# Optimization experiments

Measured on AMD Instinct MI355X. Metric: run time of the kernel, lower is better.

Reference implementation:

```python
import jax, jax.numpy as jnp
import numpy as np

H = 1024  # hid_dim


def setup_inputs() -> dict:
    key = jax.random.key(0)
    k1, k2, k3, k4 = jax.random.split(key, 4)
    B, S = 64, 2048
    dec_out = jax.random.normal(k1, (B, H), dtype=jnp.float32)
    enc_outs = jax.random.normal(k2, (S, B, H), dtype=jnp.float32)
    # GeneralScorer W_a: Linear(H, H, bias=False); torch Linear: y = x @ W.T
    W_a = jax.random.normal(k3, (H, H), dtype=jnp.float32) / np.sqrt(H)
    # linear_out: Linear(2H, H, bias=False) since scorer == 'general'
    W_out = jax.random.normal(k4, (H, 2 * H), dtype=jnp.float32) / np.sqrt(2 * H)
    return {"dec_out": dec_out, "enc_outs": enc_outs, "W_a": W_a, "W_out": W_out}


def reference(dec_out, enc_outs, W_a, W_out):
    # GeneralScorer: project query then dot with each encoder state
    q = dec_out @ W_a.T                               # [B, H]
    scores = jnp.einsum('sbh,bh->bs', enc_outs, q)    # [B, S]
    weights = jax.nn.softmax(scores, axis=1)          # [B, S]
    # context = weights @ enc_outs (per batch)
    context = jnp.einsum('bs,sbh->bh', weights, enc_outs)  # [B, H]
    context = jnp.tanh(jnp.concatenate([context, dec_out], axis=1) @ W_out.T)
    return (context, weights)
```

## Files before the change

### kernel.cpp

```cpp
#include <hip/hip_runtime.h>
#include <math.h>

#define BB 64
#define SS 2048
#define HH 1024
#define NCHUNK 16
#define CHUNK 128

#define Q_OFF    0
#define PCTX_OFF (BB * HH)
#define PML_OFF  (PCTX_OFF + BB * NCHUNK * HH)
#define CTXF_OFF (PML_OFF + BB * NCHUNK * 2)

__global__ __launch_bounds__(256) void gemm64(
    const float* __restrict__ A0, const float* __restrict__ A1,
    const float* __restrict__ W, float* __restrict__ out,
    int nchunks, int do_tanh)
{
    __shared__ float A_lds[64 * 256];
    __shared__ float W_lds[4 * 256];
    const int t  = threadIdx.x;
    const int it = blockIdx.x;
    const int b  = t & 63;
    const int il = t >> 6;
    const int K  = nchunks << 8;
    float acc = 0.f;

    for (int kc = 0; kc < nchunks; ++kc) {
        for (int idx = t; idx < 64 * 64; idx += 256) {
            const int row = idx >> 6;
            const int g   = idx & 63;
            const float* src = (kc < 4) ? (A0 + row * 1024 + kc * 256)
                                        : (A1 + row * 1024 + (kc - 4) * 256);
            float4 v = *(const float4*)(src + g * 4);
            ((float4*)A_lds)[row * 64 + (g ^ row)] = v;
        }
        for (int idx = t; idx < 1024; idx += 256) {
            const int r2 = idx >> 8;
            const int cc = idx & 255;
            W_lds[idx] = W[(size_t)(it * 4 + r2) * K + kc * 256 + cc];
        }
        __syncthreads();
        #pragma unroll 8
        for (int j4 = 0; j4 < 64; ++j4) {
            float4 a  = ((const float4*)A_lds)[b * 64 + (j4 ^ b)];
            float4 wv = ((const float4*)W_lds)[il * 64 + j4];
            acc += a.x * wv.x + a.y * wv.y + a.z * wv.z + a.w * wv.w;
        }
        __syncthreads();
    }
    if (do_tanh) acc = tanhf(acc);
    out[b * 1024 + it * 4 + il] = acc;
}

__global__ __launch_bounds__(256) void attn_partial(
    const float* __restrict__ enc, const float* __restrict__ q,
    float* __restrict__ part_ctx, float* __restrict__ part_ml,
    float* __restrict__ scores_raw)
{
    __shared__ float q_lds[HH];
    __shared__ float ctx_lds[4][HH];
    __shared__ float ml_lds[4][2];

    const int t = threadIdx.x;
    const int c = blockIdx.x;
    const int b = blockIdx.y;

    for (int i = t; i < HH / 4; i += 256)
        ((float4*)q_lds)[i] = ((const float4*)(q + b * HH))[i];
    __syncthreads();

    const int w    = t >> 6;
    const int lane = t & 63;
    float m = -INFINITY, lsum = 0.f;
    float ctx[16];
    #pragma unroll
    for (int e = 0; e < 16; ++e) ctx[e] = 0.f;

    const int RPW = CHUNK / 4;
    for (int r = 0; r < RPW; ++r) {
        const int s = c * CHUNK + w * RPW + r;
        const float* row = enc + ((size_t)s * BB + b) * HH;
        float4 v[4];
        float partial = 0.f;
        #pragma unroll
        for (int k = 0; k < 4; ++k) {
            v[k] = *(const float4*)(row + k * 256 + 4 * lane);
            float4 qv = *(const float4*)(q_lds + k * 256 + 4 * lane);
            partial += v[k].x * qv.x + v[k].y * qv.y + v[k].z * qv.z + v[k].w * qv.w;
        }
        #pragma unroll
        for (int off = 32; off; off >>= 1)
            partial += __shfl_xor(partial, off, 64);
        const float sc = partial;
        if (lane == 0) scores_raw[b * SS + s] = sc;

        if (sc > m) {
            const float scale = expf(m - sc);
            lsum *= scale;
            #pragma unroll
            for (int e = 0; e < 16; ++e) ctx[e] *= scale;
            m = sc;
        }
        const float p = expf(sc - m);
        lsum += p;
        #pragma unroll
        for (int k = 0; k < 4; ++k) {
            ctx[4 * k + 0] += p * v[k].x;
            ctx[4 * k + 1] += p * v[k].y;
            ctx[4 * k + 2] += p * v[k].z;
            ctx[4 * k + 3] += p * v[k].w;
        }
    }

    if (lane == 0) { ml_lds[w][0] = m; ml_lds[w][1] = lsum; }
    #pragma unroll
    for (int k = 0; k < 4; ++k)
        *(float4*)&ctx_lds[w][k * 256 + 4 * lane] =
            make_float4(ctx[4 * k + 0], ctx[4 * k + 1], ctx[4 * k + 2], ctx[4 * k + 3]);
    __syncthreads();

    const float m0 = ml_lds[0][0], m1 = ml_lds[1][0], m2 = ml_lds[2][0], m3 = ml_lds[3][0];
    const float mb = fmaxf(fmaxf(m0, m1), fmaxf(m2, m3));
    const float f0 = expf(m0 - mb), f1 = expf(m1 - mb), f2 = expf(m2 - mb), f3 = expf(m3 - mb);
    const float lb = f0 * ml_lds[0][1] + f1 * ml_lds[1][1] + f2 * ml_lds[2][1] + f3 * ml_lds[3][1];

    float4 a0 = ((const float4*)&ctx_lds[0][0])[t];
    float4 a1 = ((const float4*)&ctx_lds[1][0])[t];
    float4 a2 = ((const float4*)&ctx_lds[2][0])[t];
    float4 a3 = ((const float4*)&ctx_lds[3][0])[t];
    float4 o;
    o.x = f0 * a0.x + f1 * a1.x + f2 * a2.x + f3 * a3.x;
    o.y = f0 * a0.y + f1 * a1.y + f2 * a2.y + f3 * a3.y;
    o.z = f0 * a0.z + f1 * a1.z + f2 * a2.z + f3 * a3.z;
    o.w = f0 * a0.w + f1 * a1.w + f2 * a2.w + f3 * a3.w;
    ((float4*)(part_ctx + ((size_t)b * NCHUNK + c) * HH))[t] = o;
    if (t == 0) {
        part_ml[(b * NCHUNK + c) * 2 + 0] = mb;
        part_ml[(b * NCHUNK + c) * 2 + 1] = lb;
    }
}

__global__ __launch_bounds__(256) void attn_combine(
    const float* __restrict__ part_ctx, const float* __restrict__ part_ml,
    float* __restrict__ ctx_final, float* __restrict__ wts)
{
    const int b = blockIdx.x;
    const int t = threadIdx.x;
    __shared__ float mls[NCHUNK][2];
    for (int i = t; i < NCHUNK * 2; i += 256)
        ((float*)mls)[i] = part_ml[b * NCHUNK * 2 + i];
    __syncthreads();

    float M = -INFINITY;
    #pragma unroll
    for (int c2 = 0; c2 < NCHUNK; ++c2) M = fmaxf(M, mls[c2][0]);
    float f[NCHUNK];
    float L = 0.f;
    #pragma unroll
    for (int c2 = 0; c2 < NCHUNK; ++c2) {
        f[c2] = expf(mls[c2][0] - M);
        L += f[c2] * mls[c2][1];
    }
    const float inv = 1.0f / L;

    float4 acc = make_float4(0.f, 0.f, 0.f, 0.f);
    #pragma unroll
    for (int c2 = 0; c2 < NCHUNK; ++c2) {
        float4 v = ((const float4*)(part_ctx + ((size_t)b * NCHUNK + c2) * HH))[t];
        acc.x += f[c2] * v.x; acc.y += f[c2] * v.y;
        acc.z += f[c2] * v.z; acc.w += f[c2] * v.w;
    }
    acc.x *= inv; acc.y *= inv; acc.z *= inv; acc.w *= inv;
    ((float4*)(ctx_final + (size_t)b * HH))[t] = acc;

    for (int s = t; s < SS; s += 256)
        wts[b * SS + s] = expf(wts[b * SS + s] - M) * inv;
}

extern "C" void kernel_launch(void* const* d_in, const int* in_sizes, int n_in,
                              void* d_out, int out_size, void* d_ws, size_t ws_size,
                              hipStream_t stream)
{
    const float* dec   = (const float*)d_in[0];
    const float* enc   = (const float*)d_in[1];
    const float* W_a   = (const float*)d_in[2];
    const float* W_out = (const float*)d_in[3];
    float* out = (float*)d_out;
    float* ws  = (float*)d_ws;

    float* q         = ws + Q_OFF;
    float* part_ctx  = ws + PCTX_OFF;
    float* part_ml   = ws + PML_OFF;
    float* ctx_final = ws + CTXF_OFF;
    float* wts       = out + BB * HH;

    gemm64<<<256, 256, 0, stream>>>(dec, dec, W_a, q, 4, 0);
    attn_partial<<<dim3(NCHUNK, BB), 256, 0, stream>>>(enc, q, part_ctx, part_ml, wts);
    attn_combine<<<BB, 256, 0, stream>>>(part_ctx, part_ml, ctx_final, wts);
    gemm64<<<256, 256, 0, stream>>>(ctx_final, dec, W_out, out, 8, 1);
}
```

Before: 208.5 us.

## Split-K GEMMs, double-buffer encoder loads, and widen attention chunking

Both GEMMs move to a split-K kernel in which each thread computes four output columns. Partial sums go to workspace and are reduced in the attention kernel and in a new tanh combine kernel. The attention partial kernel now uses 32 chunks of 64 rows, processes two rows per step with register double-buffered nontemporal loads and a branchless online softmax, and the combine kernel is spread over four blocks per batch. The aim is more parallelism and better hiding of memory latency on the dominant encoder stream, at the cost of an extra launch and extra workspace traffic for the partial results.

```diff
diff --git a/kernel.cpp b/kernel.cpp
--- a/kernel.cpp
+++ b/kernel.cpp
@@ -4,57 +4,67 @@
 #define BB 64
 #define SS 2048
 #define HH 1024
-#define NCHUNK 16
-#define CHUNK 128
-
-#define Q_OFF    0
-#define PCTX_OFF (BB * HH)
+#define NCHUNK 32
+#define CHUNK 64
+#define RPW 16
+
+typedef float f4 __attribute__((ext_vector_type(4)));
+
+#define QP_OFF   0
+#define PCTX_OFF (QP_OFF + 4 * BB * HH)
 #define PML_OFF  (PCTX_OFF + BB * NCHUNK * HH)
 #define CTXF_OFF (PML_OFF + BB * NCHUNK * 2)
-
-__global__ __launch_bounds__(256) void gemm64(
+#define OP_OFF   (CTXF_OFF + BB * HH)
+
+__global__ __launch_bounds__(256) void gemm_cols16(
     const float* __restrict__ A0, const float* __restrict__ A1,
-    const float* __restrict__ W, float* __restrict__ out,
-    int nchunks, int do_tanh)
-{
-    __shared__ float A_lds[64 * 256];
-    __shared__ float W_lds[4 * 256];
-    const int t  = threadIdx.x;
-    const int it = blockIdx.x;
-    const int b  = t & 63;
-    const int il = t >> 6;
-    const int K  = nchunks << 8;
-    float acc = 0.f;
-
-    for (int kc = 0; kc < nchunks; ++kc) {
-        for (int idx = t; idx < 64 * 64; idx += 256) {
-            const int row = idx >> 6;
-            const int g   = idx & 63;
-            const float* src = (kc < 4) ? (A0 + row * 1024 + kc * 256)
-                                        : (A1 + row * 1024 + (kc - 4) * 256);
-            float4 v = *(const float4*)(src + g * 4);
-            ((float4*)A_lds)[row * 64 + (g ^ row)] = v;
-        }
-        for (int idx = t; idx < 1024; idx += 256) {
-            const int r2 = idx >> 8;
-            const int cc = idx & 255;
-            W_lds[idx] = W[(size_t)(it * 4 + r2) * K + kc * 256 + cc];
+    const float* __restrict__ W, float* __restrict__ out_part,
+    int KTOT, int CPB)
+{
+    __shared__ f4 A_lds[64 * 32];
+    __shared__ f4 W_lds[16 * 32];
+    const int t    = threadIdx.x;
+    const int tile = blockIdx.x;
+    const int spl  = blockIdx.y;
+    const int b    = t & 63;
+    const int cg   = t >> 6;
+    float acc[4] = {0.f, 0.f, 0.f, 0.f};
+
+    for (int kk = 0; kk < CPB; ++kk) {
+        const int kc = spl * CPB + kk;
+        #pragma unroll
+        for (int i = 0; i < 8; ++i) {
+            const int idx = t + i * 256;
+            const int row = idx >> 5, g = idx & 31;
+            const float* src = (kc < 8) ? (A0 + row * 1024 + kc * 128)
+                                        : (A1 + row * 1024 + (kc - 8) * 128);
+            A_lds[row * 32 + (g ^ (row & 31))] = *(const f4*)(src + g * 4);
+        }
+        #pragma unroll
+        for (int i = 0; i < 2; ++i) {
+            const int idx = t + i * 256;
+            const int r = idx >> 5, g = idx & 31;
+            W_lds[r * 32 + g] =
+                *(const f4*)(W + (size_t)(tile * 16 + r) * KTOT + kc * 128 + g * 4);
         }
         __syncthreads();
         #pragma unroll 8
-        for (int j4 = 0; j4 < 64; ++j4) {
-            float4 a  = ((const float4*)A_lds)[b * 64 + (j4 ^ b)];
-            float4 wv = ((const float4*)W_lds)[il * 64 + j4];
-            acc += a.x * wv.x + a.y * wv.y + a.z * wv.z + a.w * wv.w;
+        for (int j4 = 0; j4 < 32; ++j4) {
+            const f4 a = A_lds[b * 32 + (j4 ^ (b & 31))];
+            #pragma unroll
+            for (int cix = 0; cix < 4; ++cix) {
+                const f4 wv = W_lds[(cg * 4 + cix) * 32 + j4];
+                acc[cix] += a.x * wv.x + a.y * wv.y + a.z * wv.z + a.w * wv.w;
+            }
         }
         __syncthreads();
     }
-    if (do_tanh) acc = tanhf(acc);
-    out[b * 1024 + it * 4 + il] = acc;
-}
-
-__global__ __launch_bounds__(256) void attn_partial(
-    const float* __restrict__ enc, const float* __restrict__ q,
+    float* op = out_part + ((size_t)spl * BB + b) * HH + tile * 16 + cg * 4;
+    *(f4*)op = (f4){acc[0], acc[1], acc[2], acc[3]};
+}
+
+__global__ __launch_bounds__(256, 4) void attn_partial(
+    const float* __restrict__ enc, const float* __restrict__ qp,
     float* __restrict__ part_ctx, float* __restrict__ part_ml,
     float* __restrict__ scores_raw)
 {
@@ -66,58 +76,80 @@
     const int c = blockIdx.x;
     const int b = blockIdx.y;
 
-    for (int i = t; i < HH / 4; i += 256)
-        ((float4*)q_lds)[i] = ((const float4*)(q + b * HH))[i];
+    {
+        const f4 v = ((const f4*)(qp + (size_t)b * HH))[t]
+                   + ((const f4*)(qp + 65536 + (size_t)b * HH))[t]
+                   + ((const f4*)(qp + 131072 + (size_t)b * HH))[t]
+                   + ((const f4*)(qp + 196608 + (size_t)b * HH))[t];
+        ((f4*)q_lds)[t] = v;
+    }
     __syncthreads();
 
     const int w    = t >> 6;
     const int lane = t & 63;
+    const size_t RS = (size_t)BB * HH;
+    const float* rp = enc + ((size_t)(c * CHUNK + w * RPW) * BB + b) * HH + 4 * lane;
+
+    f4 cur0[4], cur1[4], nxt0[4], nxt1[4];
+    #pragma unroll
+    for (int k = 0; k < 4; ++k) {
+        cur0[k] = __builtin_nontemporal_load((const f4*)(rp + k * 256));
+        cur1[k] = __builtin_nontemporal_load((const f4*)(rp + RS + k * 256));
+    }
+
     float m = -INFINITY, lsum = 0.f;
-    float ctx[16];
-    #pragma unroll
-    for (int e = 0; e < 16; ++e) ctx[e] = 0.f;
-
-    const int RPW = CHUNK / 4;
-    for (int r = 0; r < RPW; ++r) {
-        const int s = c * CHUNK + w * RPW + r;
-        const float* row = enc + ((size_t)s * BB + b) * HH;
-        float4 v[4];
-        float partial = 0.f;
+    f4 ctxv[4];
+    #pragma unroll
+    for (int k = 0; k < 4; ++k) ctxv[k] = (f4)0.f;
+
+    #pragma unroll
+    for (int r = 0; r < RPW; r += 2) {
+        if (r + 2 < RPW) {
+            const float* np = rp + 2 * RS;
+            #pragma unroll
+            for (int k = 0; k < 4; ++k) {
+                nxt0[k] = __builtin_nontemporal_load((const f4*)(np + k * 256));
+                nxt1[k] = __builtin_nontemporal_load((const f4*)(np + RS + k * 256));
+            }
+        }
+        float d0 = 0.f, d1 = 0.f;
         #pragma unroll
         for (int k = 0; k < 4; ++k) {
-            v[k] = *(const float4*)(row + k * 256 + 4 * lane);
-            float4 qv = *(const float4*)(q_lds + k * 256 + 4 * lane);
-            partial += v[k].x * qv.x + v[k].y * qv.y + v[k].z * qv.z + v[k].w * qv.w;
-        }
-        #pragma unroll
-        for (int off = 32; off; off >>= 1)
-            partial += __shfl_xor(partial, off, 64);
-        const float sc = partial;
-        if (lane == 0) scores_raw[b * SS + s] = sc;
-
-        if (sc > m) {
-            const float scale = expf(m - sc);
-            lsum *= scale;
+            const f4 qv = *(const f4*)(q_lds + k * 256 + 4 * lane);
+            d0 += cur0[k].x * qv.x + cur0[k].y * qv.y + cur0[k].z * qv.z + cur0[k].w * qv.w;
+            d1 += cur1[k].x * qv.x + cur1[k].y * qv.y + cur1[k].z * qv.z + cur1[k].w * qv.w;
+        }
+        #pragma unroll
+        for (int off = 32; off; off >>= 1) {
+            d0 += __shfl_xor(d0, off, 64);
+            d1 += __shfl_xor(d1, off, 64);
+        }
+        if (lane == 0) {
+            const int s = c * CHUNK + w * RPW + r;
+            scores_raw[b * SS + s]     = d0;
+            scores_raw[b * SS + s + 1] = d1;
+        }
+        const float mx = fmaxf(d0, d1);
+        const float nm = fmaxf(m, mx);
+        const float sc = expf(m - nm);
+        const float p0 = expf(d0 - nm);
+        const float p1 = expf(d1 - nm);
+        lsum = lsum * sc + p0 + p1;
+        m = nm;
+        #pragma unroll
+        for (int k = 0; k < 4; ++k)
+            ctxv[k] = ctxv[k] * sc + p0 * cur0[k] + p1 * cur1[k];
+        if (r + 2 < RPW) {
             #pragma unroll
-            for (int e = 0; e < 16; ++e) ctx[e] *= scale;
-            m = sc;
-        }
-        const float p = expf(sc - m);
-        lsum += p;
-        #pragma unroll
-        for (int k = 0; k < 4; ++k) {
-            ctx[4 * k + 0] += p * v[k].x;
-            ctx[4 * k + 1] += p * v[k].y;
-            ctx[4 * k + 2] += p * v[k].z;
-            ctx[4 * k + 3] += p * v[k].w;
+            for (int k = 0; k < 4; ++k) { cur0[k] = nxt0[k]; cur1[k] = nxt1[k]; }
+            rp += 2 * RS;
         }
     }
 
     if (lane == 0) { ml_lds[w][0] = m; ml_lds[w][1] = lsum; }
     #pragma unroll
     for (int k = 0; k < 4; ++k)
-        *(float4*)&ctx_lds[w][k * 256 + 4 * lane] =
-            make_float4(ctx[4 * k + 0], ctx[4 * k + 1], ctx[4 * k + 2], ctx[4 * k + 3]);
+        *(f4*)&ctx_lds[w][k * 256 + 4 * lane] = ctxv[k];
     __syncthreads();
 
     const float m0 = ml_lds[0][0], m1 = ml_lds[1][0], m2 = ml_lds[2][0], m3 = ml_lds[3][0];
@@ -125,16 +157,12 @@
     const float f0 = expf(m0 - mb), f1 = expf(m1 - mb), f2 = expf(m2 - mb), f3 = expf(m3 - mb);
     const float lb = f0 * ml_lds[0][1] + f1 * ml_lds[1][1] + f2 * ml_lds[2][1] + f3 * ml_lds[3][1];
 
-    float4 a0 = ((const float4*)&ctx_lds[0][0])[t];
-    float4 a1 = ((const float4*)&ctx_lds[1][0])[t];
-    float4 a2 = ((const float4*)&ctx_lds[2][0])[t];
-    float4 a3 = ((const float4*)&ctx_lds[3][0])[t];
-    float4 o;
-    o.x = f0 * a0.x + f1 * a1.x + f2 * a2.x + f3 * a3.x;
-    o.y = f0 * a0.y + f1 * a1.y + f2 * a2.y + f3 * a3.y;
-    o.z = f0 * a0.z + f1 * a1.z + f2 * a2.z + f3 * a3.z;
-    o.w = f0 * a0.w + f1 * a1.w + f2 * a2.w + f3 * a3.w;
-    ((float4*)(part_ctx + ((size_t)b * NCHUNK + c) * HH))[t] = o;
+    const f4 a0 = ((const f4*)&ctx_lds[0][0])[t];
+    const f4 a1 = ((const f4*)&ctx_lds[1][0])[t];
+    const f4 a2 = ((const f4*)&ctx_lds[2][0])[t];
+    const f4 a3 = ((const f4*)&ctx_lds[3][0])[t];
+    const f4 o = f0 * a0 + f1 * a1 + f2 * a2 + f3 * a3;
+    ((f4*)(part_ctx + ((size_t)(b * NCHUNK + c)) * HH))[t] = o;
     if (t == 0) {
         part_ml[(b * NCHUNK + c) * 2 + 0] = mb;
         part_ml[(b * NCHUNK + c) * 2 + 1] = lb;
@@ -145,37 +173,49 @@
     const float* __restrict__ part_ctx, const float* __restrict__ part_ml,
     float* __restrict__ ctx_final, float* __restrict__ wts)
 {
-    const int b = blockIdx.x;
-    const int t = threadIdx.x;
-    __shared__ float mls[NCHUNK][2];
-    for (int i = t; i < NCHUNK * 2; i += 256)
-        ((float*)mls)[i] = part_ml[b * NCHUNK * 2 + i];
+    const int b = blockIdx.x, quad = blockIdx.y, t = threadIdx.x;
+    __shared__ float mls[NCHUNK * 2];
+    if (t < NCHUNK * 2) mls[t] = part_ml[b * NCHUNK * 2 + t];
     __syncthreads();
 
     float M = -INFINITY;
     #pragma unroll
-    for (int c2 = 0; c2 < NCHUNK; ++c2) M = fmaxf(M, mls[c2][0]);
+    for (int cc = 0; cc < NCHUNK; ++cc) M = fmaxf(M, mls[2 * cc]);
+    float L = 0.f;
     float f[NCHUNK];
-    float L = 0.f;
-    #pragma unroll
-    for (int c2 = 0; c2 < NCHUNK; ++c2) {
-        f[c2] = expf(mls[c2][0] - M);
-        L += f[c2] * mls[c2][1];
+    #pragma unroll
+    for (int cc = 0; cc < NCHUNK; ++cc) {
+        f[cc] = expf(mls[2 * cc] - M);
+        L += f[cc] * mls[2 * cc + 1];
     }
     const float inv = 1.0f / L;
 
-    float4 acc = make_float4(0.f, 0.f, 0.f, 0.f);
-    #pragma unroll
-    for (int c2 = 0; c2 < NCHUNK; ++c2) {
-        float4 v = ((const float4*)(part_ctx + ((size_t)b * NCHUNK + c2) * HH))[t];
-        acc.x += f[c2] * v.x; acc.y += f[c2] * v.y;
-        acc.z += f[c2] * v.z; acc.w += f[c2] * v.w;
-    }
-    acc.x *= inv; acc.y *= inv; acc.z *= inv; acc.w *= inv;
-    ((float4*)(ctx_final + (size_t)b * HH))[t] = acc;
-
-    for (int s = t; s < SS; s += 256)
-        wts[b * SS + s] = expf(wts[b * SS + s] - M) * inv;
+    if (t < 64) {
+        f4 acc = (f4)0.f;
+        #pragma unroll
+        for (int cc = 0; cc < NCHUNK; ++cc) {
+            const f4 v = ((const f4*)(part_ctx + ((size_t)(b * NCHUNK + cc)) * HH + quad * 256))[t];
+            acc += f[cc] * v;
+        }
+        ((f4*)(ctx_final + (size_t)b * HH + quad * 256))[t] = acc * inv;
+    }
+    const int s0 = quad * 512 + 2 * t;
+    const float w0 = wts[b * SS + s0], w1 = wts[b * SS + s0 + 1];
+    wts[b * SS + s0]     = expf(w0 - M) * inv;
+    wts[b * SS + s0 + 1] = expf(w1 - M) * inv;
+}
+
+__global__ __launch_bounds__(256) void gemm2_combine(
+    const float* __restrict__ op, float* __restrict__ out)
+{
+    const int i = blockIdx.x * 256 + threadIdx.x;
+    f4 a = (f4)0.f;
+    #pragma unroll
+    for (int sp = 0; sp < 8; ++sp)
+        a += ((const f4*)(op + (size_t)sp * BB * HH))[i];
+    f4 r;
+    r.x = tanhf(a.x); r.y = tanhf(a.y); r.z = tanhf(a.z); r.w = tanhf(a.w);
+    ((f4*)out)[i] = r;
 }
 
 extern "C" void kernel_launch(void* const* d_in, const int* in_sizes, int n_in,
@@ -189,14 +229,16 @@
     float* out = (float*)d_out;
     float* ws  = (float*)d_ws;
 
-    float* q         = ws + Q_OFF;
+    float* q_part    = ws + QP_OFF;
     float* part_ctx  = ws + PCTX_OFF;
     float* part_ml   = ws + PML_OFF;
     float* ctx_final = ws + CTXF_OFF;
+    float* o_part    = ws + OP_OFF;
     float* wts       = out + BB * HH;
 
-    gemm64<<<256, 256, 0, stream>>>(dec, dec, W_a, q, 4, 0);
-    attn_partial<<<dim3(NCHUNK, BB), 256, 0, stream>>>(enc, q, part_ctx, part_ml, wts);
-    attn_combine<<<BB, 256, 0, stream>>>(part_ctx, part_ml, ctx_final, wts);
-    gemm64<<<256, 256, 0, stream>>>(ctx_final, dec, W_out, out, 8, 1);
-}
+    gemm_cols16<<<dim3(64, 4), 256, 0, stream>>>(dec, dec, W_a, q_part, 1024, 2);
+    attn_partial<<<dim3(NCHUNK, BB), 256, 0, stream>>>(enc, q_part, part_ctx, part_ml, wts);
+    attn_combine<<<dim3(BB, 4), 256, 0, stream>>>(part_ctx, part_ml, ctx_final, wts);
+    gemm_cols16<<<dim3(64, 8), 256, 0, stream>>>(ctx_final, dec, W_out, o_part, 2048, 2);
+    gemm2_combine<<<64, 256, 0, stream>>>(o_part, out);
+}
```

Result: slower. 300.4 us (+44.1%).
